# Kernel optimization log

Hardware: AMD Instinct MI355X
Metric: run time of the kernel (lower is better)

## Reference

```python
import jax, jax.numpy as jnp
import numpy as np

B, S, IN, HID, OUT = 8, 4096, 128, 128, 1

def setup_inputs() -> dict:
    key = jax.random.key(0)
    ks = jax.random.split(key, 16)
    xav = lambda k, i, o: jax.random.normal(k, (i, o), jnp.float32) * np.sqrt(2.0 / (i + o))
    return {
        'x': jax.random.normal(ks[0], (B, S, IN), jnp.float32),
        'm1': xav(ks[1], IN, HID), 'b1': jnp.zeros((1, 1, HID), jnp.float32),
        'm2': xav(ks[2], HID, HID), 'b2': jnp.zeros((1, 1, HID), jnp.float32),
        'wq': xav(ks[3], HID, HID), 'wk': xav(ks[4], HID, HID), 'wv': xav(ks[5], HID, HID),
        'ml0': xav(ks[6], 128, 64), 'bl0': jnp.zeros((1, 1, 64), jnp.float32),
        'ml1': xav(ks[7], 64, 32), 'bl1': jnp.zeros((1, 1, 32), jnp.float32),
        'm3': xav(ks[8], 32, OUT), 'b3': jnp.zeros((1, 1, OUT), jnp.float32),
        'atten_size': 5,
    }

def reference(x, m1, b1, m2, b2, wq, wk, wv, ml0, bl0, ml1, bl1, m3, b3, atten_size):
    a = atten_size
    h = jax.nn.relu(x @ m1 + b1)
    h = jax.nn.relu(h @ m2 + b2)            # [B,S,H]
    vals = h @ wv
    pad_cfg = ((0, 0), (a, a), (0, 0))
    padded = jnp.pad(h, pad_cfg)
    padded_v = jnp.pad(vals, pad_cfg)
    # window gather via roll, matching torch.roll(padded, k, 1) for k=-a..a, then slice
    x_nei = jnp.stack([jnp.roll(padded, k, axis=1) for k in range(-a, a + 1)], axis=2)[:, a:-a]   # [B,S,W,H]
    v_nei = jnp.stack([jnp.roll(padded_v, k, axis=1) for k in range(-a, a + 1)], axis=2)[:, a:-a]
    keys = x_nei @ wk                        # [B,S,W,H]
    query = h @ wq                           # [B,S,H]
    scale = 1.0 / np.sqrt(float(HID))
    dot = jnp.einsum('bswh,bsh->bsw', keys, query) * scale
    atten_w = jax.nn.softmax(dot, axis=2)    # [B,S,W]
    o = jnp.einsum('bsw,bswh->bsh', atten_w, v_nei)
    o = jax.nn.relu(o @ ml0 + bl0)
    o = jax.nn.relu(o @ ml1 + bl1)
    o = jax.nn.sigmoid(o @ m3 + b3)          # [B,S,OUT]
    return (o, atten_w)
```

## Files before the change

kernel.cpp:

```cpp
#include <hip/hip_runtime.h>
#include <math.h>

#define SEQ 4096
#define NB 8
#define CHUNK 64
#define HALO 5
#define WIN 11
#define MROWS 80
#define AROWS 74
#define HSTR 136
#define NT 512
#define CNT 256

typedef short s16x8 __attribute__((ext_vector_type(8)));
typedef float f32x4 __attribute__((ext_vector_type(4)));

__device__ __forceinline__ unsigned short f2bf(float f) {
    unsigned u = __builtin_bit_cast(unsigned, f);
    u += 0x7fffu + ((u >> 16) & 1u);
    return (unsigned short)(u >> 16);
}

#define OFF_M1  0
#define OFF_M2  16384
#define OFF_WQ  32768
#define OFF_WK  49152
#define OFF_WV  65536
#define OFF_ML0 81920
#define OFF_ML1 90112
#define WS_ELEMS 92160

__global__ void convert_weights(const float* __restrict__ m1, const float* __restrict__ m2,
                                const float* __restrict__ wq, const float* __restrict__ wk,
                                const float* __restrict__ wv, const float* __restrict__ ml0,
                                const float* __restrict__ ml1, unsigned short* __restrict__ ws)
{
    int idx = blockIdx.x * CNT + threadIdx.x;
    if (idx < OFF_ML0) {
        int seg = idx >> 14;
        int r = idx & 16383;
        int n = r >> 7, k = r & 127;
        const float* w = (seg == 0) ? m1 : (seg == 1) ? m2 : (seg == 2) ? wq
                       : (seg == 3) ? wk : wv;
        ws[idx] = f2bf(w[k * 128 + n]);
    } else if (idx < OFF_ML1) {
        int r = idx - OFF_ML0;
        int n = r >> 7, k = r & 127;
        ws[idx] = f2bf(ml0[k * 64 + n]);
    } else if (idx < WS_ELEMS) {
        int r = idx - OFF_ML1;
        int n = r >> 6, k = r & 63;
        ws[idx] = f2bf(ml1[k * 32 + n]);
    }
}

template<int MT, bool RELU, bool BIAS>
__device__ __forceinline__ void gemm128(const unsigned short* __restrict__ src,
                                        const unsigned short* __restrict__ wt,
                                        const float* __restrict__ bias,
                                        unsigned short* __restrict__ dst,
                                        int l15, int hi, int wave)
{
    f32x4 acc[MT];
    #pragma unroll
    for (int i = 0; i < MT; ++i) acc[i] = (f32x4){0.f, 0.f, 0.f, 0.f};

    const unsigned short* wrow = wt + (wave * 16 + l15) * 128 + hi * 8;
    const unsigned short* arow = src + l15 * HSTR + hi * 8;
    #pragma unroll
    for (int ks = 0; ks < 4; ++ks) {
        s16x8 b = *(const s16x8*)(wrow + ks * 32);
        #pragma unroll
        for (int rt = 0; rt < MT; ++rt) {
            s16x8 a = *(const s16x8*)(arow + (rt * 16) * HSTR + ks * 32);
            acc[rt] = __builtin_amdgcn_mfma_f32_16x16x32_bf16(a, b, acc[rt], 0, 0, 0);
        }
    }
    const int c = wave * 16 + l15;
    const float bb = BIAS ? bias[c] : 0.f;
    #pragma unroll
    for (int rt = 0; rt < MT; ++rt)
        #pragma unroll
        for (int j = 0; j < 4; ++j) {
            float v = acc[rt][j] + bb;
            if (RELU) v = fmaxf(v, 0.f);
            dst[(rt * 16 + hi * 4 + j) * HSTR + c] = f2bf(v);
        }
}

__global__ __launch_bounds__(NT, 4)
void ExLRestSelfAtten_mfma(const float* __restrict__ x,
                           const float* __restrict__ b1, const float* __restrict__ b2,
                           const float* __restrict__ bl0, const float* __restrict__ bl1,
                           const float* __restrict__ m3, const float* __restrict__ b3,
                           const unsigned short* __restrict__ wsw,
                           float* __restrict__ out0, float* __restrict__ attw)
{
    __shared__ __align__(16) unsigned short bufA[MROWS * HSTR];
    __shared__ __align__(16) unsigned short bufB[MROWS * HSTR];
    __shared__ __align__(16) unsigned short qbuf[CHUNK * HSTR];

    float* sbuf = (float*)qbuf;
    float* saw  = (float*)qbuf + 2304;
    unsigned short* h64 = bufB;
    float* fbuf = (float*)(bufB + 4608);

    const int t = threadIdx.x;
    const int lane = t & 63, wave = t >> 6;
    const int l15 = lane & 15, hi = lane >> 4;
    const int bx = blockIdx.x;
    const int b = bx >> 6;
    const int cstart = (bx & 63) * CHUNK;

    const float* xb = x + (size_t)b * SEQ * 128;
    for (int idx = t; idx < MROWS * 32; idx += NT) {
        int r = idx >> 5, k4 = (idx & 31) << 2;
        int p = cstart - HALO + r;
        float4 v = make_float4(0.f, 0.f, 0.f, 0.f);
        if (r < AROWS && p >= 0 && p < SEQ) v = *(const float4*)(xb + (size_t)p * 128 + k4);
        ushort4 o;
        o.x = f2bf(v.x); o.y = f2bf(v.y); o.z = f2bf(v.z); o.w = f2bf(v.w);
        *(ushort4*)(bufA + r * HSTR + k4) = o;
    }
    __syncthreads();

    gemm128<5, true, true>(bufA, wsw + OFF_M1, b1, bufB, l15, hi, wave);
    __syncthreads();
    gemm128<5, true, true>(bufB, wsw + OFF_M2, b2, bufA, l15, hi, wave);
    __syncthreads();

    gemm128<4, false, false>(bufA + HALO * HSTR, wsw + OFF_WQ, nullptr, qbuf, l15, hi, wave);
    gemm128<5, false, false>(bufA, wsw + OFF_WK, nullptr, bufB, l15, hi, wave);
    __syncthreads();

    const int rt = wave >> 1, kk = wave & 1, kt = rt + kk;
    f32x4 sacc = (f32x4){0.f, 0.f, 0.f, 0.f};
    #pragma unroll
    for (int ks = 0; ks < 4; ++ks) {
        s16x8 a  = *(const s16x8*)(qbuf + (rt * 16 + l15) * HSTR + ks * 32 + hi * 8);
        s16x8 kf = *(const s16x8*)(bufB + (kt * 16 + l15) * HSTR + ks * 32 + hi * 8);
        sacc = __builtin_amdgcn_mfma_f32_16x16x32_bf16(a, kf, sacc, 0, 0, 0);
    }
    __syncthreads();

    #pragma unroll
    for (int j = 0; j < 4; ++j)
        sbuf[rt * 576 + (hi * 4 + j) * 36 + kk * 16 + l15] = sacc[j] * 0.08838834764831845f;
    gemm128<5, false, false>(bufA, wsw + OFF_WV, nullptr, bufB, l15, hi, wave);
    __syncthreads();

    if (t < CHUNK) {
        const int base = (t >> 4) * 576 + (t & 15) * 36 + (t & 15) + 10;
        float d[WIN], mx = -1e30f;
        #pragma unroll
        for (int w = 0; w < WIN; ++w) { d[w] = sbuf[base - w]; mx = fmaxf(mx, d[w]); }
        float sum = 0.f;
        #pragma unroll
        for (int w = 0; w < WIN; ++w) { d[w] = __expf(d[w] - mx); sum += d[w]; }
        float inv = 1.f / sum;
        #pragma unroll
        for (int w = 0; w < WIN; ++w) saw[t * WIN + w] = d[w] * inv;
    }
    __syncthreads();

    for (int idx = t; idx < CHUNK * 16; idx += NT) {
        int s = idx >> 4, c0 = (idx & 15) << 3;
        float acc[8] = {0.f, 0.f, 0.f, 0.f, 0.f, 0.f, 0.f, 0.f};
        #pragma unroll
        for (int w = 0; w < WIN; ++w) {
            float aw = saw[s * WIN + w];
            uint4 u = *(const uint4*)(bufB + (s + 10 - w) * HSTR + c0);
            unsigned uu[4] = {u.x, u.y, u.z, u.w};
            #pragma unroll
            for (int q = 0; q < 4; ++q) {
                acc[2 * q]     = fmaf(aw, __builtin_bit_cast(float, uu[q] << 16), acc[2 * q]);
                acc[2 * q + 1] = fmaf(aw, __builtin_bit_cast(float, uu[q] & 0xffff0000u), acc[2 * q + 1]);
            }
        }
        unsigned p0 = f2bf(acc[0]) | ((unsigned)f2bf(acc[1]) << 16);
        unsigned p1 = f2bf(acc[2]) | ((unsigned)f2bf(acc[3]) << 16);
        unsigned p2 = f2bf(acc[4]) | ((unsigned)f2bf(acc[5]) << 16);
        unsigned p3 = f2bf(acc[6]) | ((unsigned)f2bf(acc[7]) << 16);
        *(uint4*)(bufA + s * HSTR + c0) = make_uint4(p0, p1, p2, p3);
    }
    {
        float* ab = attw + (size_t)(b * SEQ + cstart) * WIN;
        for (int idx = t; idx < CHUNK * WIN; idx += NT) ab[idx] = saw[idx];
    }
    __syncthreads();

    {
        const int ct4 = wave & 3;
        f32x4 acc[2] = {(f32x4){0.f,0.f,0.f,0.f}, (f32x4){0.f,0.f,0.f,0.f}};
        #pragma unroll
        for (int ks = 0; ks < 4; ++ks) {
            s16x8 bfr = *(const s16x8*)(wsw + OFF_ML0 + (ct4 * 16 + l15) * 128 + ks * 32 + hi * 8);
            #pragma unroll
            for (int q = 0; q < 2; ++q) {
                int rr = (wave >> 2) + 2 * q;
                s16x8 a = *(const s16x8*)(bufA + (rr * 16 + l15) * HSTR + ks * 32 + hi * 8);
                acc[q] = __builtin_amdgcn_mfma_f32_16x16x32_bf16(a, bfr, acc[q], 0, 0, 0);
            }
        }
        int c = ct4 * 16 + l15;
        float bb = bl0[c];
        #pragma unroll
        for (int q = 0; q < 2; ++q)
            #pragma unroll
            for (int j = 0; j < 4; ++j)
                h64[(((wave >> 2) + 2 * q) * 16 + hi * 4 + j) * 72 + c] = f2bf(fmaxf(acc[q][j] + bb, 0.f));
    }
    __syncthreads();

    {
        const int rt2 = wave >> 1, ct2 = wave & 1;
        f32x4 acc = (f32x4){0.f, 0.f, 0.f, 0.f};
        #pragma unroll
        for (int ks = 0; ks < 2; ++ks) {
            s16x8 a   = *(const s16x8*)(h64 + (rt2 * 16 + l15) * 72 + ks * 32 + hi * 8);
            s16x8 bfr = *(const s16x8*)(wsw + OFF_ML1 + (ct2 * 16 + l15) * 64 + ks * 32 + hi * 8);
            acc = __builtin_amdgcn_mfma_f32_16x16x32_bf16(a, bfr, acc, 0, 0, 0);
        }
        int c = ct2 * 16 + l15;
        float bb = bl1[c];
        #pragma unroll
        for (int j = 0; j < 4; ++j)
            fbuf[(rt2 * 16 + hi * 4 + j) * 36 + c] = fmaxf(acc[j] + bb, 0.f);
    }
    __syncthreads();

    if (t < CHUNK) {
        float acc = b3[0];
        #pragma unroll
        for (int k = 0; k < 32; ++k) acc = fmaf(fbuf[t * 36 + k], m3[k], acc);
        out0[(size_t)b * SEQ + cstart + t] = 1.f / (1.f + __expf(-acc));
    }
}

extern "C" void kernel_launch(void* const* d_in, const int* in_sizes, int n_in,
                              void* d_out, int out_size, void* d_ws, size_t ws_size,
                              hipStream_t stream)
{
    const float* x   = (const float*)d_in[0];
    const float* m1  = (const float*)d_in[1];
    const float* b1  = (const float*)d_in[2];
    const float* m2  = (const float*)d_in[3];
    const float* b2  = (const float*)d_in[4];
    const float* wq  = (const float*)d_in[5];
    const float* wk  = (const float*)d_in[6];
    const float* wv  = (const float*)d_in[7];
    const float* ml0 = (const float*)d_in[8];
    const float* bl0 = (const float*)d_in[9];
    const float* ml1 = (const float*)d_in[10];
    const float* bl1 = (const float*)d_in[11];
    const float* m3  = (const float*)d_in[12];
    const float* b3  = (const float*)d_in[13];

    float* out0 = (float*)d_out;
    float* attw = out0 + (size_t)NB * SEQ;

    unsigned short* wsw = (unsigned short*)d_ws;
    convert_weights<<<(WS_ELEMS + CNT - 1) / CNT, CNT, 0, stream>>>(m1, m2, wq, wk, wv, ml0, ml1, wsw);
    ExLRestSelfAtten_mfma<<<NB * (SEQ / CHUNK), NT, 0, stream>>>(
        x, b1, b2, bl0, bl1, m3, b3, wsw, out0, attw);
}
```

Baseline: 30.19 us.

## Fold Wq·Wkᵀ into one weight, drop key GEMM, prefetch weights into registers

Precomputes a combined Wq·Wkᵀ matrix, pre-scaled by 1/sqrt(H), in the weight-conversion kernel. Queries then become h·(WqWkᵀ) and scores are dotted directly against h, so the per-block key GEMM over 80 rows goes away. Weight fragments for later GEMMs are also loaded into registers ahead of the preceding GEMM to hide global latency, and the score and attention buffers get their own shared-memory arrays. The trade-offs are higher register pressure and an extra bf16 rounding of the combined matrix, which slightly changes numerics.

```diff
diff --git a/kernel.cpp b/kernel.cpp
--- a/kernel.cpp
+++ b/kernel.cpp
@@ -1,4 +1,5 @@
 #include <hip/hip_runtime.h>
+#include <hip/hip_bf16.h>
 #include <math.h>
 
 #define SEQ 4096
@@ -16,19 +17,17 @@
 typedef float f32x4 __attribute__((ext_vector_type(4)));
 
 __device__ __forceinline__ unsigned short f2bf(float f) {
-    unsigned u = __builtin_bit_cast(unsigned, f);
-    u += 0x7fffu + ((u >> 16) & 1u);
-    return (unsigned short)(u >> 16);
+    return __builtin_bit_cast(unsigned short, __float2bfloat16(f));
 }
 
 #define OFF_M1  0
 #define OFF_M2  16384
-#define OFF_WQ  32768
-#define OFF_WK  49152
-#define OFF_WV  65536
-#define OFF_ML0 81920
-#define OFF_ML1 90112
-#define WS_ELEMS 92160
+#define OFF_WQK 32768
+#define OFF_WV  49152
+#define OFF_ML0 65536
+#define OFF_ML1 73728
+#define CONV_A  59392
+#define WS_ELEMS 75776
 
 __global__ void convert_weights(const float* __restrict__ m1, const float* __restrict__ m2,
                                 const float* __restrict__ wq, const float* __restrict__ wk,
@@ -36,46 +35,64 @@
                                 const float* __restrict__ ml1, unsigned short* __restrict__ ws)
 {
     int idx = blockIdx.x * CNT + threadIdx.x;
-    if (idx < OFF_ML0) {
-        int seg = idx >> 14;
-        int r = idx & 16383;
-        int n = r >> 7, k = r & 127;
-        const float* w = (seg == 0) ? m1 : (seg == 1) ? m2 : (seg == 2) ? wq
-                       : (seg == 3) ? wk : wv;
-        ws[idx] = f2bf(w[k * 128 + n]);
-    } else if (idx < OFF_ML1) {
-        int r = idx - OFF_ML0;
-        int n = r >> 7, k = r & 127;
-        ws[idx] = f2bf(ml0[k * 64 + n]);
+    if (idx < 16384) {
+        ws[OFF_M1 + idx] = f2bf(m1[(idx & 127) * 128 + (idx >> 7)]);
+    } else if (idx < 32768) {
+        int r = idx - 16384;
+        ws[OFF_M2 + r] = f2bf(m2[(r & 127) * 128 + (r >> 7)]);
+    } else if (idx < 49152) {
+        int r = idx - 32768;
+        ws[OFF_WV + r] = f2bf(wv[(r & 127) * 128 + (r >> 7)]);
+    } else if (idx < 57344) {
+        int r = idx - 49152;
+        ws[OFF_ML0 + r] = f2bf(ml0[(r & 127) * 64 + (r >> 7)]);
+    } else if (idx < CONV_A) {
+        int r = idx - 57344;
+        ws[OFF_ML1 + r] = f2bf(ml1[(r & 63) * 32 + (r >> 6)]);
     } else if (idx < WS_ELEMS) {
-        int r = idx - OFF_ML1;
-        int n = r >> 6, k = r & 63;
-        ws[idx] = f2bf(ml1[k * 32 + n]);
-    }
+        int r = idx - CONV_A;
+        int d = r >> 7, e = r & 127;
+        const float4* qa = (const float4*)(wq + e * 128);
+        const float4* ka = (const float4*)(wk + d * 128);
+        float a0 = 0.f, a1 = 0.f, a2 = 0.f, a3 = 0.f;
+        #pragma unroll
+        for (int c = 0; c < 32; ++c) {
+            float4 A = qa[c], B = ka[c];
+            a0 = fmaf(A.x, B.x, a0); a1 = fmaf(A.y, B.y, a1);
+            a2 = fmaf(A.z, B.z, a2); a3 = fmaf(A.w, B.w, a3);
+        }
+        ws[OFF_WQK + r] = f2bf((a0 + a1 + a2 + a3) * 0.08838834764831845f);
+    }
+}
+
+__device__ __forceinline__ void loadB4(s16x8 d[4], const unsigned short* __restrict__ wt,
+                                       int ct, int l15, int hi)
+{
+    const unsigned short* p = wt + (ct * 16 + l15) * 128 + hi * 8;
+    d[0] = *(const s16x8*)(p);
+    d[1] = *(const s16x8*)(p + 32);
+    d[2] = *(const s16x8*)(p + 64);
+    d[3] = *(const s16x8*)(p + 96);
 }
 
 template<int MT, bool RELU, bool BIAS>
-__device__ __forceinline__ void gemm128(const unsigned short* __restrict__ src,
-                                        const unsigned short* __restrict__ wt,
-                                        const float* __restrict__ bias,
-                                        unsigned short* __restrict__ dst,
-                                        int l15, int hi, int wave)
+__device__ __forceinline__ void gemmS(const unsigned short* __restrict__ src,
+                                      const s16x8 bf[4],
+                                      const float* __restrict__ bias,
+                                      unsigned short* __restrict__ dst,
+                                      int l15, int hi, int wave)
 {
     f32x4 acc[MT];
     #pragma unroll
     for (int i = 0; i < MT; ++i) acc[i] = (f32x4){0.f, 0.f, 0.f, 0.f};
-
-    const unsigned short* wrow = wt + (wave * 16 + l15) * 128 + hi * 8;
     const unsigned short* arow = src + l15 * HSTR + hi * 8;
     #pragma unroll
-    for (int ks = 0; ks < 4; ++ks) {
-        s16x8 b = *(const s16x8*)(wrow + ks * 32);
+    for (int ks = 0; ks < 4; ++ks)
         #pragma unroll
         for (int rt = 0; rt < MT; ++rt) {
-            s16x8 a = *(const s16x8*)(arow + (rt * 16) * HSTR + ks * 32);
-            acc[rt] = __builtin_amdgcn_mfma_f32_16x16x32_bf16(a, b, acc[rt], 0, 0, 0);
-        }
-    }
+            s16x8 a = *(const s16x8*)(arow + rt * 16 * HSTR + ks * 32);
+            acc[rt] = __builtin_amdgcn_mfma_f32_16x16x32_bf16(a, bf[ks], acc[rt], 0, 0, 0);
+        }
     const int c = wave * 16 + l15;
     const float bb = BIAS ? bias[c] : 0.f;
     #pragma unroll
@@ -99,11 +116,11 @@
     __shared__ __align__(16) unsigned short bufA[MROWS * HSTR];
     __shared__ __align__(16) unsigned short bufB[MROWS * HSTR];
     __shared__ __align__(16) unsigned short qbuf[CHUNK * HSTR];
-
-    float* sbuf = (float*)qbuf;
-    float* saw  = (float*)qbuf + 2304;
-    unsigned short* h64 = bufB;
-    float* fbuf = (float*)(bufB + 4608);
+    __shared__ __align__(16) float sbuf[4 * 16 * 36];
+    __shared__ __align__(16) float saw [CHUNK * WIN];
+
+    unsigned short* h64 = bufA;
+    float* fbuf = (float*)(bufA + 4608);
 
     const int t = threadIdx.x;
     const int lane = t & 63, wave = t >> 6;
@@ -111,6 +128,9 @@
     const int bx = blockIdx.x;
     const int b = bx >> 6;
     const int cstart = (bx & 63) * CHUNK;
+
+    s16x8 wA[4], wB[4], wml0[4], wml1[2];
+    loadB4(wA, wsw + OFF_M1, wave, l15, hi);
 
     const float* xb = x + (size_t)b * SEQ * 128;
     for (int idx = t; idx < MROWS * 32; idx += NT) {
@@ -124,29 +144,38 @@
     }
     __syncthreads();
 
-    gemm128<5, true, true>(bufA, wsw + OFF_M1, b1, bufB, l15, hi, wave);
-    __syncthreads();
-    gemm128<5, true, true>(bufB, wsw + OFF_M2, b2, bufA, l15, hi, wave);
-    __syncthreads();
-
-    gemm128<4, false, false>(bufA + HALO * HSTR, wsw + OFF_WQ, nullptr, qbuf, l15, hi, wave);
-    gemm128<5, false, false>(bufA, wsw + OFF_WK, nullptr, bufB, l15, hi, wave);
-    __syncthreads();
-
-    const int rt = wave >> 1, kk = wave & 1, kt = rt + kk;
-    f32x4 sacc = (f32x4){0.f, 0.f, 0.f, 0.f};
-    #pragma unroll
-    for (int ks = 0; ks < 4; ++ks) {
-        s16x8 a  = *(const s16x8*)(qbuf + (rt * 16 + l15) * HSTR + ks * 32 + hi * 8);
-        s16x8 kf = *(const s16x8*)(bufB + (kt * 16 + l15) * HSTR + ks * 32 + hi * 8);
-        sacc = __builtin_amdgcn_mfma_f32_16x16x32_bf16(a, kf, sacc, 0, 0, 0);
-    }
-    __syncthreads();
-
-    #pragma unroll
-    for (int j = 0; j < 4; ++j)
-        sbuf[rt * 576 + (hi * 4 + j) * 36 + kk * 16 + l15] = sacc[j] * 0.08838834764831845f;
-    gemm128<5, false, false>(bufA, wsw + OFF_WV, nullptr, bufB, l15, hi, wave);
+    loadB4(wB, wsw + OFF_M2, wave, l15, hi);
+    gemmS<5, true, true>(bufA, wA, b1, bufB, l15, hi, wave);
+    __syncthreads();
+
+    loadB4(wA, wsw + OFF_WQK, wave, l15, hi);
+    gemmS<5, true, true>(bufB, wB, b2, bufA, l15, hi, wave);
+    __syncthreads();
+
+    loadB4(wB, wsw + OFF_WV, wave, l15, hi);
+    gemmS<4, false, false>(bufA + HALO * HSTR, wA, nullptr, qbuf, l15, hi, wave);
+    loadB4(wml0, wsw + OFF_ML0, wave & 3, l15, hi);
+    gemmS<5, false, false>(bufA, wB, nullptr, bufB, l15, hi, wave);
+    __syncthreads();
+
+    {
+        const unsigned short* p1 = wsw + OFF_ML1 + ((wave & 1) * 16 + l15) * 64 + hi * 8;
+        wml1[0] = *(const s16x8*)(p1);
+        wml1[1] = *(const s16x8*)(p1 + 32);
+    }
+    {
+        const int rt = wave >> 1, kk = wave & 1, kt = rt + kk;
+        f32x4 sacc = (f32x4){0.f, 0.f, 0.f, 0.f};
+        #pragma unroll
+        for (int ks = 0; ks < 4; ++ks) {
+            s16x8 a  = *(const s16x8*)(qbuf + (rt * 16 + l15) * HSTR + ks * 32 + hi * 8);
+            s16x8 hb = *(const s16x8*)(bufA + (kt * 16 + l15) * HSTR + ks * 32 + hi * 8);
+            sacc = __builtin_amdgcn_mfma_f32_16x16x32_bf16(a, hb, sacc, 0, 0, 0);
+        }
+        #pragma unroll
+        for (int j = 0; j < 4; ++j)
+            sbuf[rt * 576 + (hi * 4 + j) * 36 + kk * 16 + l15] = sacc[j];
+    }
     __syncthreads();
 
     if (t < CHUNK) {
@@ -181,7 +210,7 @@
         unsigned p1 = f2bf(acc[2]) | ((unsigned)f2bf(acc[3]) << 16);
         unsigned p2 = f2bf(acc[4]) | ((unsigned)f2bf(acc[5]) << 16);
         unsigned p3 = f2bf(acc[6]) | ((unsigned)f2bf(acc[7]) << 16);
-        *(uint4*)(bufA + s * HSTR + c0) = make_uint4(p0, p1, p2, p3);
+        *(uint4*)(qbuf + s * HSTR + c0) = make_uint4(p0, p1, p2, p3);
     }
     {
         float* ab = attw + (size_t)(b * SEQ + cstart) * WIN;
@@ -193,15 +222,13 @@
         const int ct4 = wave & 3;
         f32x4 acc[2] = {(f32x4){0.f,0.f,0.f,0.f}, (f32x4){0.f,0.f,0.f,0.f}};
         #pragma unroll
-        for (int ks = 0; ks < 4; ++ks) {
-            s16x8 bfr = *(const s16x8*)(wsw + OFF_ML0 + (ct4 * 16 + l15) * 128 + ks * 32 + hi * 8);
+        for (int ks = 0; ks < 4; ++ks)
             #pragma unroll
             for (int q = 0; q < 2; ++q) {
                 int rr = (wave >> 2) + 2 * q;
-                s16x8 a = *(const s16x8*)(bufA + (rr * 16 + l15) * HSTR + ks * 32 + hi * 8);
-                acc[q] = __builtin_amdgcn_mfma_f32_16x16x32_bf16(a, bfr, acc[q], 0, 0, 0);
+                s16x8 a = *(const s16x8*)(qbuf + (rr * 16 + l15) * HSTR + ks * 32 + hi * 8);
+                acc[q] = __builtin_amdgcn_mfma_f32_16x16x32_bf16(a, wml0[ks], acc[q], 0, 0, 0);
             }
-        }
         int c = ct4 * 16 + l15;
         float bb = bl0[c];
         #pragma unroll
@@ -217,9 +244,8 @@
         f32x4 acc = (f32x4){0.f, 0.f, 0.f, 0.f};
         #pragma unroll
         for (int ks = 0; ks < 2; ++ks) {
-            s16x8 a   = *(const s16x8*)(h64 + (rt2 * 16 + l15) * 72 + ks * 32 + hi * 8);
-            s16x8 bfr = *(const s16x8*)(wsw + OFF_ML1 + (ct2 * 16 + l15) * 64 + ks * 32 + hi * 8);
-            acc = __builtin_amdgcn_mfma_f32_16x16x32_bf16(a, bfr, acc, 0, 0, 0);
+            s16x8 a = *(const s16x8*)(h64 + (rt2 * 16 + l15) * 72 + ks * 32 + hi * 8);
+            acc = __builtin_amdgcn_mfma_f32_16x16x32_bf16(a, wml1[ks], acc, 0, 0, 0);
         }
         int c = ct2 * 16 + l15;
         float bb = bl1[c];
@@ -260,7 +286,8 @@
     float* attw = out0 + (size_t)NB * SEQ;
 
     unsigned short* wsw = (unsigned short*)d_ws;
-    convert_weights<<<(WS_ELEMS + CNT - 1) / CNT, CNT, 0, stream>>>(m1, m2, wq, wk, wv, ml0, ml1, wsw);
+    convert_weights<<<(WS_ELEMS + CNT - 1) / CNT, CNT, 0, stream>>>(
+        m1, m2, wq, wk, wv, ml0, ml1, wsw);
     ExLRestSelfAtten_mfma<<<NB * (SEQ / CHUNK), NT, 0, stream>>>(
         x, b1, b2, bl0, bl1, m3, b3, wsw, out0, attw);
 }
```

New measurement: 27.18 us. -10.0%, faster.
